# Optimization experiments

Measured on AMD Instinct MI355X. Metric: run time of the kernel, lower is better.

Reference implementation:

```python
import jax, jax.numpy as jnp
import numpy as np

B, G, K, KD = 16384, 17, 12, 16      # batch, games, kicks/game, kick feature dim
DK, DM, H, T = 16, 32, 2, 4          # d_kick, d_model, n_attn_heads, n_targets
SD, H1, H2, HH = 64, 256, 128, 32    # static_dim, backbone hidden dims, head hidden
AO = H * DM                          # attention output dim = 64
EPS = 1e-5
NEG_INF = float('-inf')


def setup_inputs() -> dict:
    ks = jax.random.split(jax.random.key(0), 18)
    n = lambda i, s, sc=0.05: jax.random.normal(ks[i], s, jnp.float32) * sc
    x_static = jax.random.normal(ks[0], (B, SD), jnp.float32)
    x_kicks = jax.random.normal(ks[1], (B, G, K, KD), jnp.float32)
    # masks: True = real game / kick; force position 0 valid so no row is fully padded
    outer_mask = jax.random.bernoulli(ks[2], 0.9, (B, G)).at[:, 0].set(True)
    inner_mask = jax.random.bernoulli(ks[3], 0.85, (B, G, K)).at[:, :, 0].set(True)
    return dict(
        x_static=x_static, x_kicks=x_kicks,
        W_ke=n(4, (KD, DK)), b_ke=jnp.zeros((DK,), jnp.float32),
        q_inner=n(5, (1, DK), 0.02),
        W_ge=n(6, (DK, DM)), b_ge=jnp.zeros((DM,), jnp.float32),
        pos_emb=n(7, (G, DM), 0.02),
        q_outer=n(8, (T * H, DM), 0.02),
        log_temp=jnp.zeros((T,), jnp.float32),
        ln_g=jnp.ones((T, AO), jnp.float32), ln_b=jnp.zeros((T, AO), jnp.float32),
        W1=n(9, (SD, H1)), b1=jnp.zeros((H1,), jnp.float32),
        g1=jnp.ones((H1,), jnp.float32), be1=jnp.zeros((H1,), jnp.float32),
        m1=n(10, (H1,)), v1=jax.random.uniform(ks[11], (H1,), jnp.float32) + 0.5,
        W2=n(12, (H1, H2)), b2=jnp.zeros((H2,), jnp.float32),
        g2=jnp.ones((H2,), jnp.float32), be2=jnp.zeros((H2,), jnp.float32),
        m2=n(13, (H2,)), v2=jax.random.uniform(ks[14], (H2,), jnp.float32) + 0.5,
        Wh1=n(15, (T, H2 + AO, HH)), bh1=jnp.zeros((T, HH), jnp.float32),
        Wh2=n(16, (T, HH)), bh2=jnp.zeros((T,), jnp.float32),
        outer_mask=outer_mask, inner_mask=inner_mask)


def _forward(x_static, x_kicks, W_ke, b_ke, q_inner, W_ge, b_ge, pos_emb,
             q_outer, log_temp, ln_g, ln_b, W1, b1, g1, be1, m1, v1,
             W2, b2, g2, be2, m2, v2, Wh1, bh1, Wh2, bh2,
             outer_mask, inner_mask):
    # kick encoder: Linear -> ReLU, [B,G,K,KD] -> [B,G,K,DK]
    kick_enc = jax.nn.relu(jnp.einsum('bgkd,de->bgke', x_kicks, W_ke) + b_ke)
    # inner AttentionPool: single learned query over kicks within each game
    ai = jnp.einsum('d,bgkd->bgk', q_inner[0], kick_enc) * (DK ** -0.5)
    ai = jnp.where(inner_mask, ai, NEG_INF)
    wi = jnp.nan_to_num(jax.nn.softmax(ai, axis=-1))       # all-masked rows -> 0
    per_game = jnp.einsum('bgk,bgkd->bgd', wi, kick_enc)   # [B,G,DK]
    # game encoder + learned positional embedding
    encoded = jax.nn.relu(per_game @ W_ge + b_ge) + pos_emb[None]  # [B,G,DM]
    # outer AttentionPool: T*H learned queries over games, per-target temperature
    ao = jnp.einsum('qd,bgd->bqg', q_outer, encoded) * (DM ** -0.5)
    ao = ao * jnp.repeat(jnp.exp(-log_temp), H)[None, :, None]
    ao = jnp.where(outer_mask[:, None, :], ao, NEG_INF)
    wo = jnp.nan_to_num(jax.nn.softmax(ao, axis=-1))
    pooled = jnp.einsum('bqg,bgd->bqd', wo, encoded).reshape(-1, T, AO)  # [B,T,64]
    # per-target LayerNorm on history vector
    mu = pooled.mean(-1, keepdims=True)
    var = ((pooled - mu) ** 2).mean(-1, keepdims=True)
    hist = (pooled - mu) * jax.lax.rsqrt(var + EPS) * ln_g[None] + ln_b[None]
    # backbone: Linear -> BatchNorm(eval) -> ReLU, x2 (dropout = identity in eval)
    z = jax.nn.relu((x_static @ W1 + b1 - m1) * jax.lax.rsqrt(v1 + EPS) * g1 + be1)
    z = jax.nn.relu((z @ W2 + b2 - m2) * jax.lax.rsqrt(v2 + EPS) * g2 + be2)
    # per-target heads on [shared_static ; history_vec]
    head_in = jnp.concatenate(
        [jnp.broadcast_to(z[:, None, :], (z.shape[0], T, H2)), hist], axis=-1)  # [B,T,192]
    h = jax.nn.relu(jnp.einsum('btd,tdh->bth', head_in, Wh1) + bh1[None])
    out = jnp.einsum('bth,th->bt', h, Wh2) + bh2[None]
    return jnp.maximum(out, 0.0)  # all targets non-negative (clamp, not softplus)


def reference(x_static, x_kicks, W_ke, b_ke, q_inner, W_ge, b_ge, pos_emb,
              q_outer, log_temp, ln_g, ln_b, W1, b1, g1, be1, m1, v1,
              W2, b2, g2, be2, m2, v2, Wh1, bh1, Wh2, bh2,
              outer_mask, inner_mask):
    return _forward(x_static, x_kicks, W_ke, b_ke, q_inner, W_ge, b_ge, pos_emb,
                    q_outer, log_temp, ln_g, ln_b, W1, b1, g1, be1, m1, v1,
                    W2, b2, g2, be2, m2, v2, Wh1, bh1, Wh2, bh2,
                    outer_mask, inner_mask)
```

## Files before the change

### kernel.cpp

```cpp
#include <hip/hip_runtime.h>
#include <math.h>

#define NEGM (-1e30f)

typedef __fp16 f16x4 __attribute__((ext_vector_type(4)));
typedef __fp16 f16x2 __attribute__((ext_vector_type(2)));
typedef float  f32x4 __attribute__((ext_vector_type(4)));

__device__ __forceinline__ float4 ld4(const float* p) { return *(const float4*)p; }
__device__ __forceinline__ void fma4(float4& a, float s, const float4 w) {
    a.x += s * w.x; a.y += s * w.y; a.z += s * w.z; a.w += s * w.w;
}

__global__ __launch_bounds__(64) void hist_kernel(
    const float* __restrict__ x_kicks,
    const float* __restrict__ W_ke, const float* __restrict__ b_ke,
    const float* __restrict__ q_inner,
    const float* __restrict__ W_ge, const float* __restrict__ b_ge,
    const float* __restrict__ pos_emb, const float* __restrict__ q_outer,
    const float* __restrict__ log_temp,
    const float* __restrict__ ln_g, const float* __restrict__ ln_b,
    const int* __restrict__ outer_mask, const int* __restrict__ inner_mask,
    float* __restrict__ hist)
{
    __shared__ float s_wge[512];
    __shared__ float s_qout[256];
    __shared__ float pg[17 * 20];
    __shared__ float enc[17 * 36];
    __shared__ float ao[136];
    __shared__ float s_S[20];

    const int lane = threadIdx.x;
    const int b    = blockIdx.x;
    const int jcol = lane & 15;
    const int g    = lane >> 4;
    const int kb   = g * 4;

    *(float4*)&s_wge[lane * 4]       = ld4(W_ge + lane * 4);
    *(float4*)&s_wge[256 + lane * 4] = ld4(W_ge + 256 + lane * 4);
    *(float4*)&s_qout[lane * 4]      = ld4(q_outer + lane * 4);

    f16x4 bw;
    #pragma unroll
    for (int jj = 0; jj < 4; ++jj)
        bw[jj] = (__fp16)W_ke[(kb + jj) * 16 + jcol];
    const float bias = b_ke[jcol];
    const f32x4 cinit = {bias, bias, bias, bias};
    const float qv = q_inner[jcol];

    const float* xb = x_kicks + (size_t)b * 204 * 16;
    const int*   mb = inner_mask + (size_t)b * 204;

    f32x4 PG   = {0.f, 0.f, 0.f, 0.f};
    f32x4 PG16 = {0.f, 0.f, 0.f, 0.f};
    float Sacc = 0.f, S16 = 0.f;

    #pragma unroll
    for (int t = 0; t < 12; ++t) {
        float4 xv = ld4(xb + (16 * t + jcol) * 16 + kb);
        f16x2 xlo = __builtin_amdgcn_cvt_pkrtz(xv.x, xv.y);
        f16x2 xhi = __builtin_amdgcn_cvt_pkrtz(xv.z, xv.w);
        f16x4 ax; ax[0] = xlo[0]; ax[1] = xlo[1]; ax[2] = xhi[0]; ax[3] = xhi[1];

        int4 mv = *(const int4*)(mb + 16 * t + 4 * g);

        f32x4 D1 = __builtin_amdgcn_mfma_f32_16x16x16f16(ax, bw, cinit, 0, 0, 0);
        #pragma unroll
        for (int jj = 0; jj < 4; ++jj) D1[jj] = fmaxf(D1[jj], 0.f);

        f32x4 ps;
        #pragma unroll
        for (int jj = 0; jj < 4; ++jj) ps[jj] = D1[jj] * qv;
        #pragma unroll
        for (int o = 1; o < 16; o <<= 1) {
            ps[0] += __shfl_xor(ps[0], o);
            ps[1] += __shfl_xor(ps[1], o);
            ps[2] += __shfl_xor(ps[2], o);
            ps[3] += __shfl_xor(ps[3], o);
        }

        f16x4 aw;
        #pragma unroll
        for (int jj = 0; jj < 4; ++jj) {
            int kk = 16 * t + 4 * g + jj;
            int mk = (jj == 0) ? mv.x : (jj == 1) ? mv.y : (jj == 2) ? mv.z : mv.w;
            float e = mk ? __expf(ps[jj] * 0.25f) : 0.f;
            float w = (kk / 12 == jcol) ? e : 0.f;
            aw[jj] = (__fp16)w;
            Sacc += w;
        }

        f16x2 elo = __builtin_amdgcn_cvt_pkrtz(D1[0], D1[1]);
        f16x2 ehi = __builtin_amdgcn_cvt_pkrtz(D1[2], D1[3]);
        f16x4 be; be[0] = elo[0]; be[1] = elo[1]; be[2] = ehi[0]; be[3] = ehi[1];

        PG = __builtin_amdgcn_mfma_f32_16x16x16f16(aw, be, PG, 0, 0, 0);
    }

    {
        int kidx = 192 + jcol;
        int kc = (kidx < 204) ? kidx : 203;
        float4 xv = ld4(xb + kc * 16 + kb);
        f16x2 xlo = __builtin_amdgcn_cvt_pkrtz(xv.x, xv.y);
        f16x2 xhi = __builtin_amdgcn_cvt_pkrtz(xv.z, xv.w);
        f16x4 ax; ax[0] = xlo[0]; ax[1] = xlo[1]; ax[2] = xhi[0]; ax[3] = xhi[1];

        int km = 192 + 4 * g;
        int kmc = (km <= 200) ? km : 200;
        int4 mv = *(const int4*)(mb + kmc);

        f32x4 D1 = __builtin_amdgcn_mfma_f32_16x16x16f16(ax, bw, cinit, 0, 0, 0);
        #pragma unroll
        for (int jj = 0; jj < 4; ++jj) D1[jj] = fmaxf(D1[jj], 0.f);

        f32x4 ps;
        #pragma unroll
        for (int jj = 0; jj < 4; ++jj) ps[jj] = D1[jj] * qv;
        #pragma unroll
        for (int o = 1; o < 16; o <<= 1) {
            ps[0] += __shfl_xor(ps[0], o);
            ps[1] += __shfl_xor(ps[1], o);
            ps[2] += __shfl_xor(ps[2], o);
            ps[3] += __shfl_xor(ps[3], o);
        }

        f16x4 aw2;
        #pragma unroll
        for (int jj = 0; jj < 4; ++jj) {
            int pos = 4 * g + jj;
            int mk = (jj == 0) ? mv.x : (jj == 1) ? mv.y : (jj == 2) ? mv.z : mv.w;
            bool valid = (pos < 12) && mk;
            float e = valid ? __expf(ps[jj] * 0.25f) : 0.f;
            float w = (jcol == 0) ? e : 0.f;
            aw2[jj] = (__fp16)w;
            S16 += w;
        }

        f16x2 elo = __builtin_amdgcn_cvt_pkrtz(D1[0], D1[1]);
        f16x2 ehi = __builtin_amdgcn_cvt_pkrtz(D1[2], D1[3]);
        f16x4 be; be[0] = elo[0]; be[1] = elo[1]; be[2] = ehi[0]; be[3] = ehi[1];

        PG16 = __builtin_amdgcn_mfma_f32_16x16x16f16(aw2, be, PG16, 0, 0, 0);
    }

    Sacc += __shfl_xor(Sacc, 16);
    Sacc += __shfl_xor(Sacc, 32);
    S16 += __shfl_xor(S16, 16);
    S16 += __shfl_xor(S16, 32);

    if (lane < 16) s_S[lane] = Sacc;
    if (lane == 0) s_S[16] = S16;
    __syncthreads();

    #pragma unroll
    for (int jj = 0; jj < 4; ++jj) {
        int game = kb + jj;
        pg[game * 20 + jcol] = PG[jj] * (1.f / s_S[game]);
    }
    if (lane < 16) pg[16 * 20 + lane] = PG16[0] * (1.f / s_S[16]);
    __syncthreads();

    for (int t = lane; t < 136; t += 64) {
        const int gg = t >> 3, dq = t & 7;
        float4 acc = ld4(b_ge + dq * 4);
        #pragma unroll
        for (int i = 0; i < 16; ++i) {
            float pv = pg[gg * 20 + i];
            fma4(acc, pv, *(float4*)&s_wge[i * 32 + dq * 4]);
        }
        float4 pe = ld4(pos_emb + gg * 32 + dq * 4);
        acc.x = fmaxf(acc.x, 0.f) + pe.x; acc.y = fmaxf(acc.y, 0.f) + pe.y;
        acc.z = fmaxf(acc.z, 0.f) + pe.z; acc.w = fmaxf(acc.w, 0.f) + pe.w;
        *(float4*)&enc[gg * 36 + dq * 4] = acc;
    }
    __syncthreads();

    for (int t = lane; t < 136; t += 64) {
        const int q = t / 17, gg = t - q * 17;
        float4 acc = {0.f, 0.f, 0.f, 0.f};
        #pragma unroll
        for (int i4 = 0; i4 < 8; ++i4) {
            float4 ev = *(float4*)&enc[gg * 36 + i4 * 4];
            float4 qvv = *(float4*)&s_qout[q * 32 + i4 * 4];
            acc.x += ev.x * qvv.x; acc.y += ev.y * qvv.y;
            acc.z += ev.z * qvv.z; acc.w += ev.w * qvv.w;
        }
        float sv = (acc.x + acc.y) + (acc.z + acc.w);
        sv *= 0.17677669529663687f * __expf(-log_temp[q >> 1]);
        ao[t] = outer_mask[b * 17 + gg] ? sv : NEGM;
    }
    __syncthreads();

    {
        const int q = lane >> 3, j = lane & 7;
        float s0 = ao[q * 17 + j];
        float s1 = ao[q * 17 + j + 8];
        float s2 = (j == 0) ? ao[q * 17 + 16] : NEGM;
        float mx = fmaxf(fmaxf(s0, s1), s2);
        mx = fmaxf(mx, __shfl_xor(mx, 1));
        mx = fmaxf(mx, __shfl_xor(mx, 2));
        mx = fmaxf(mx, __shfl_xor(mx, 4));
        float e0 = __expf(s0 - mx), e1 = __expf(s1 - mx);
        float e2 = (j == 0) ? __expf(s2 - mx) : 0.f;
        float ssum = e0 + e1 + e2;
        ssum += __shfl_xor(ssum, 1);
        ssum += __shfl_xor(ssum, 2);
        ssum += __shfl_xor(ssum, 4);
        float inv = 1.f / ssum;
        ao[q * 17 + j] = e0 * inv;
        ao[q * 17 + j + 8] = e1 * inv;
        if (j == 0) ao[q * 17 + 16] = e2 * inv;
    }
    __syncthreads();

    {
        const int q = lane >> 3, dq = lane & 7;
        float4 acc = {0.f, 0.f, 0.f, 0.f};
        #pragma unroll
        for (int gg = 0; gg < 17; ++gg) {
            float w = ao[q * 17 + gg];
            fma4(acc, w, *(float4*)&enc[gg * 36 + dq * 4]);
        }
        float sv = (acc.x + acc.y) + (acc.z + acc.w);
        sv += __shfl_xor(sv, 1); sv += __shfl_xor(sv, 2);
        sv += __shfl_xor(sv, 4); sv += __shfl_xor(sv, 8);
        float mu = sv * 0.015625f;
        float4 d;
        d.x = acc.x - mu; d.y = acc.y - mu; d.z = acc.z - mu; d.w = acc.w - mu;
        float v = (d.x * d.x + d.y * d.y) + (d.z * d.z + d.w * d.w);
        v += __shfl_xor(v, 1); v += __shfl_xor(v, 2);
        v += __shfl_xor(v, 4); v += __shfl_xor(v, 8);
        float rs = rsqrtf(v * 0.015625f + 1e-5f);
        float4 gam = ld4(ln_g + lane * 4);
        float4 bet = ld4(ln_b + lane * 4);
        float4 res;
        res.x = d.x * rs * gam.x + bet.x; res.y = d.y * rs * gam.y + bet.y;
        res.z = d.z * rs * gam.z + bet.z; res.w = d.w * rs * gam.w + bet.w;
        *(float4*)&hist[(size_t)b * 256 + lane * 4] = res;
    }
}

__global__ __launch_bounds__(256) void backbone_kernel(
    const float* __restrict__ x_static,
    const float* __restrict__ W1, const float* __restrict__ b1,
    const float* __restrict__ g1, const float* __restrict__ be1,
    const float* __restrict__ m1, const float* __restrict__ v1,
    const float* __restrict__ W2, const float* __restrict__ b2,
    const float* __restrict__ g2, const float* __restrict__ be2,
    const float* __restrict__ m2, const float* __restrict__ v2,
    const float* __restrict__ Wh1, const float* __restrict__ bh1,
    const float* __restrict__ Wh2, const float* __restrict__ bh2,
    const float* __restrict__ hist, float* __restrict__ out)
{
    __shared__ float s_x[16 * 64];
    __shared__ float s_z1[16 * 256];
    __shared__ float s_z2[16 * 132];

    const int tid = threadIdx.x;
    const int row0 = blockIdx.x * 16;

    *(float4*)&s_x[tid * 4] = ld4(x_static + (size_t)row0 * 64 + tid * 4);
    __syncthreads();

    {
        const int col = tid;
        float acc[16];
        #pragma unroll
        for (int r = 0; r < 16; ++r) acc[r] = 0.f;
        for (int k4 = 0; k4 < 16; ++k4) {
            float w0 = W1[(k4 * 4 + 0) * 256 + col];
            float w1 = W1[(k4 * 4 + 1) * 256 + col];
            float w2 = W1[(k4 * 4 + 2) * 256 + col];
            float w3 = W1[(k4 * 4 + 3) * 256 + col];
            #pragma unroll
            for (int r = 0; r < 16; ++r) {
                float4 xv = *(float4*)&s_x[r * 64 + k4 * 4];
                acc[r] += xv.x * w0 + xv.y * w1 + xv.z * w2 + xv.w * w3;
            }
        }
        float sc = rsqrtf(v1[col] + 1e-5f) * g1[col];
        float off = b1[col] - m1[col];
        float bb = be1[col];
        #pragma unroll
        for (int r = 0; r < 16; ++r)
            s_z1[r * 256 + col] = fmaxf((acc[r] + off) * sc + bb, 0.f);
    }
    __syncthreads();

    {
        const int col = tid & 127;
        const int r0 = (tid >> 7) * 8;
        float acc[8];
        #pragma unroll
        for (int r = 0; r < 8; ++r) acc[r] = 0.f;
        for (int k4 = 0; k4 < 64; ++k4) {
            float w0 = W2[(k4 * 4 + 0) * 128 + col];
            float w1 = W2[(k4 * 4 + 1) * 128 + col];
            float w2 = W2[(k4 * 4 + 2) * 128 + col];
            float w3 = W2[(k4 * 4 + 3) * 128 + col];
            #pragma unroll
            for (int r = 0; r < 8; ++r) {
                float4 zv = *(float4*)&s_z1[(r0 + r) * 256 + k4 * 4];
                acc[r] += zv.x * w0 + zv.y * w1 + zv.z * w2 + zv.w * w3;
            }
        }
        float sc = rsqrtf(v2[col] + 1e-5f) * g2[col];
        float off = b2[col] - m2[col];
        float bb = be2[col];
        #pragma unroll
        for (int r = 0; r < 8; ++r)
            s_z2[(r0 + r) * 132 + col] = fmaxf((acc[r] + off) * sc + bb, 0.f);
    }
    __syncthreads();

    {
        const int p = tid >> 2;
        const int gl = tid & 3;
        const int row = p >> 2;
        const int tgt = p & 3;
        const int j0 = gl * 8;

        float acc[8];
        #pragma unroll
        for (int j = 0; j < 8; ++j) acc[j] = bh1[tgt * 32 + j0 + j];

        const float* w1p = Wh1 + (size_t)tgt * 192 * 32 + j0;
        for (int d4 = 0; d4 < 32; ++d4) {
            float4 zv = *(float4*)&s_z2[row * 132 + d4 * 4];
            #pragma unroll
            for (int c = 0; c < 4; ++c) {
                float v = (c == 0) ? zv.x : (c == 1) ? zv.y : (c == 2) ? zv.z : zv.w;
                float4 a = ld4(w1p + (d4 * 4 + c) * 32);
                float4 bq = ld4(w1p + (d4 * 4 + c) * 32 + 4);
                acc[0] += v * a.x;  acc[1] += v * a.y;  acc[2] += v * a.z;  acc[3] += v * a.w;
                acc[4] += v * bq.x; acc[5] += v * bq.y; acc[6] += v * bq.z; acc[7] += v * bq.w;
            }
        }
        const float* hp = hist + (size_t)(row0 + row) * 256 + tgt * 64;
        const float* w1q = w1p + 128 * 32;
        for (int d4 = 0; d4 < 16; ++d4) {
            float4 hv = ld4(hp + d4 * 4);
            #pragma unroll
            for (int c = 0; c < 4; ++c) {
                float v = (c == 0) ? hv.x : (c == 1) ? hv.y : (c == 2) ? hv.z : hv.w;
                float4 a = ld4(w1q + (d4 * 4 + c) * 32);
                float4 bq = ld4(w1q + (d4 * 4 + c) * 32 + 4);
                acc[0] += v * a.x;  acc[1] += v * a.y;  acc[2] += v * a.z;  acc[3] += v * a.w;
                acc[4] += v * bq.x; acc[5] += v * bq.y; acc[6] += v * bq.z; acc[7] += v * bq.w;
            }
        }
        float ps = 0.f;
        #pragma unroll
        for (int j = 0; j < 8; ++j) ps += fmaxf(acc[j], 0.f) * Wh2[tgt * 32 + j0 + j];
        ps += __shfl_xor(ps, 1);
        ps += __shfl_xor(ps, 2);
        if (gl == 0) out[(size_t)(row0 + row) * 4 + tgt] = fmaxf(ps + bh2[tgt], 0.f);
    }
}

extern "C" void kernel_launch(void* const* d_in, const int* in_sizes, int n_in,
                              void* d_out, int out_size, void* d_ws, size_t ws_size,
                              hipStream_t stream) {
    const float* x_static = (const float*)d_in[0];
    const float* x_kicks  = (const float*)d_in[1];
    const float* W_ke     = (const float*)d_in[2];
    const float* b_ke     = (const float*)d_in[3];
    const float* q_inner  = (const float*)d_in[4];
    const float* W_ge     = (const float*)d_in[5];
    const float* b_ge     = (const float*)d_in[6];
    const float* pos_emb  = (const float*)d_in[7];
    const float* q_outer  = (const float*)d_in[8];
    const float* log_temp = (const float*)d_in[9];
    const float* ln_g     = (const float*)d_in[10];
    const float* ln_b     = (const float*)d_in[11];
    const float* W1       = (const float*)d_in[12];
    const float* b1       = (const float*)d_in[13];
    const float* g1       = (const float*)d_in[14];
    const float* be1      = (const float*)d_in[15];
    const float* m1       = (const float*)d_in[16];
    const float* v1       = (const float*)d_in[17];
    const float* W2       = (const float*)d_in[18];
    const float* b2       = (const float*)d_in[19];
    const float* g2       = (const float*)d_in[20];
    const float* be2      = (const float*)d_in[21];
    const float* m2       = (const float*)d_in[22];
    const float* v2       = (const float*)d_in[23];
    const float* Wh1      = (const float*)d_in[24];
    const float* bh1      = (const float*)d_in[25];
    const float* Wh2      = (const float*)d_in[26];
    const float* bh2      = (const float*)d_in[27];
    const int* outer_mask = (const int*)d_in[28];
    const int* inner_mask = (const int*)d_in[29];

    float* hist = (float*)d_ws;
    float* out  = (float*)d_out;

    hist_kernel<<<16384, 64, 0, stream>>>(
        x_kicks, W_ke, b_ke, q_inner, W_ge, b_ge, pos_emb, q_outer,
        log_temp, ln_g, ln_b, outer_mask, inner_mask, hist);

    backbone_kernel<<<16384 / 16, 256, 0, stream>>>(
        x_static, W1, b1, g1, be1, m1, v1, W2, b2, g2, be2, m2, v2,
        Wh1, bh1, Wh2, bh2, hist, out);
}
```

Measured before the change: 145.5 us.

## Split history kernel into MFMA pooling and outer-attention kernels

The single per-sample history kernel becomes two kernels. A pooling kernel packs four samples per 256-thread block with no shared memory and writes normalized pooled game vectors to a workspace. A second kernel packs two samples per block and runs the game encoder, outer attention and layer norm. The aim is higher occupancy and less block-scheduling overhead for the bandwidth-bound kick pass, at the cost of an extra global round-trip of about 17 MB of intermediates and one more kernel launch.

```diff
diff --git a/kernel.cpp b/kernel.cpp
--- a/kernel.cpp
+++ b/kernel.cpp
@@ -12,33 +12,20 @@
     a.x += s * w.x; a.y += s * w.y; a.z += s * w.z; a.w += s * w.w;
 }
 
-__global__ __launch_bounds__(64) void hist_kernel(
+__global__ __launch_bounds__(256, 8) void pool_kernel(
     const float* __restrict__ x_kicks,
     const float* __restrict__ W_ke, const float* __restrict__ b_ke,
     const float* __restrict__ q_inner,
-    const float* __restrict__ W_ge, const float* __restrict__ b_ge,
-    const float* __restrict__ pos_emb, const float* __restrict__ q_outer,
-    const float* __restrict__ log_temp,
-    const float* __restrict__ ln_g, const float* __restrict__ ln_b,
-    const int* __restrict__ outer_mask, const int* __restrict__ inner_mask,
-    float* __restrict__ hist)
+    const int* __restrict__ inner_mask,
+    float* __restrict__ pg_out)
 {
-    __shared__ float s_wge[512];
-    __shared__ float s_qout[256];
-    __shared__ float pg[17 * 20];
-    __shared__ float enc[17 * 36];
-    __shared__ float ao[136];
-    __shared__ float s_S[20];
-
-    const int lane = threadIdx.x;
-    const int b    = blockIdx.x;
+    const int tid  = threadIdx.x;
+    const int wid  = tid >> 6;
+    const int lane = tid & 63;
+    const int b    = blockIdx.x * 4 + wid;
     const int jcol = lane & 15;
     const int g    = lane >> 4;
     const int kb   = g * 4;
-
-    *(float4*)&s_wge[lane * 4]       = ld4(W_ge + lane * 4);
-    *(float4*)&s_wge[256 + lane * 4] = ld4(W_ge + 256 + lane * 4);
-    *(float4*)&s_qout[lane * 4]      = ld4(q_outer + lane * 4);
 
     f16x4 bw;
     #pragma unroll
@@ -51,18 +38,16 @@
     const float* xb = x_kicks + (size_t)b * 204 * 16;
     const int*   mb = inner_mask + (size_t)b * 204;
 
-    f32x4 PG   = {0.f, 0.f, 0.f, 0.f};
-    f32x4 PG16 = {0.f, 0.f, 0.f, 0.f};
+    f32x4 PG = {0,0,0,0}, PG16 = {0,0,0,0};
     float Sacc = 0.f, S16 = 0.f;
 
-    #pragma unroll
     for (int t = 0; t < 12; ++t) {
         float4 xv = ld4(xb + (16 * t + jcol) * 16 + kb);
+        int4 mv = *(const int4*)(mb + 16 * t + 4 * g);
+
         f16x2 xlo = __builtin_amdgcn_cvt_pkrtz(xv.x, xv.y);
         f16x2 xhi = __builtin_amdgcn_cvt_pkrtz(xv.z, xv.w);
-        f16x4 ax; ax[0] = xlo[0]; ax[1] = xlo[1]; ax[2] = xhi[0]; ax[3] = xhi[1];
-
-        int4 mv = *(const int4*)(mb + 16 * t + 4 * g);
+        f16x4 ax; ax[0]=xlo[0]; ax[1]=xlo[1]; ax[2]=xhi[0]; ax[3]=xhi[1];
 
         f32x4 D1 = __builtin_amdgcn_mfma_f32_16x16x16f16(ax, bw, cinit, 0, 0, 0);
         #pragma unroll
@@ -83,7 +68,7 @@
         #pragma unroll
         for (int jj = 0; jj < 4; ++jj) {
             int kk = 16 * t + 4 * g + jj;
-            int mk = (jj == 0) ? mv.x : (jj == 1) ? mv.y : (jj == 2) ? mv.z : mv.w;
+            int mk = (jj==0)?mv.x:(jj==1)?mv.y:(jj==2)?mv.z:mv.w;
             float e = mk ? __expf(ps[jj] * 0.25f) : 0.f;
             float w = (kk / 12 == jcol) ? e : 0.f;
             aw[jj] = (__fp16)w;
@@ -92,7 +77,7 @@
 
         f16x2 elo = __builtin_amdgcn_cvt_pkrtz(D1[0], D1[1]);
         f16x2 ehi = __builtin_amdgcn_cvt_pkrtz(D1[2], D1[3]);
-        f16x4 be; be[0] = elo[0]; be[1] = elo[1]; be[2] = ehi[0]; be[3] = ehi[1];
+        f16x4 be; be[0]=elo[0]; be[1]=elo[1]; be[2]=ehi[0]; be[3]=ehi[1];
 
         PG = __builtin_amdgcn_mfma_f32_16x16x16f16(aw, be, PG, 0, 0, 0);
     }
@@ -101,13 +86,13 @@
         int kidx = 192 + jcol;
         int kc = (kidx < 204) ? kidx : 203;
         float4 xv = ld4(xb + kc * 16 + kb);
-        f16x2 xlo = __builtin_amdgcn_cvt_pkrtz(xv.x, xv.y);
-        f16x2 xhi = __builtin_amdgcn_cvt_pkrtz(xv.z, xv.w);
-        f16x4 ax; ax[0] = xlo[0]; ax[1] = xlo[1]; ax[2] = xhi[0]; ax[3] = xhi[1];
-
         int km = 192 + 4 * g;
         int kmc = (km <= 200) ? km : 200;
         int4 mv = *(const int4*)(mb + kmc);
+
+        f16x2 xlo = __builtin_amdgcn_cvt_pkrtz(xv.x, xv.y);
+        f16x2 xhi = __builtin_amdgcn_cvt_pkrtz(xv.z, xv.w);
+        f16x4 ax; ax[0]=xlo[0]; ax[1]=xlo[1]; ax[2]=xhi[0]; ax[3]=xhi[1];
 
         f32x4 D1 = __builtin_amdgcn_mfma_f32_16x16x16f16(ax, bw, cinit, 0, 0, 0);
         #pragma unroll
@@ -128,7 +113,7 @@
         #pragma unroll
         for (int jj = 0; jj < 4; ++jj) {
             int pos = 4 * g + jj;
-            int mk = (jj == 0) ? mv.x : (jj == 1) ? mv.y : (jj == 2) ? mv.z : mv.w;
+            int mk = (jj==0)?mv.x:(jj==1)?mv.y:(jj==2)?mv.z:mv.w;
             bool valid = (pos < 12) && mk;
             float e = valid ? __expf(ps[jj] * 0.25f) : 0.f;
             float w = (jcol == 0) ? e : 0.f;
@@ -138,7 +123,7 @@
 
         f16x2 elo = __builtin_amdgcn_cvt_pkrtz(D1[0], D1[1]);
         f16x2 ehi = __builtin_amdgcn_cvt_pkrtz(D1[2], D1[3]);
-        f16x4 be; be[0] = elo[0]; be[1] = elo[1]; be[2] = ehi[0]; be[3] = ehi[1];
+        f16x4 be; be[0]=elo[0]; be[1]=elo[1]; be[2]=ehi[0]; be[3]=ehi[1];
 
         PG16 = __builtin_amdgcn_mfma_f32_16x16x16f16(aw2, be, PG16, 0, 0, 0);
     }
@@ -147,47 +132,89 @@
     Sacc += __shfl_xor(Sacc, 32);
     S16 += __shfl_xor(S16, 16);
     S16 += __shfl_xor(S16, 32);
-
-    if (lane < 16) s_S[lane] = Sacc;
-    if (lane == 0) s_S[16] = S16;
-    __syncthreads();
-
+    float S16all = __shfl(S16, 0);
+
+    float* op = pg_out + (size_t)b * 272;
     #pragma unroll
     for (int jj = 0; jj < 4; ++jj) {
         int game = kb + jj;
-        pg[game * 20 + jcol] = PG[jj] * (1.f / s_S[game]);
-    }
-    if (lane < 16) pg[16 * 20 + lane] = PG16[0] * (1.f / s_S[16]);
-    __syncthreads();
+        float Sg = __shfl(Sacc, game);
+        op[game * 16 + jcol] = PG[jj] * (1.f / Sg);
+    }
+    if (lane < 16) op[256 + lane] = PG16[0] * (1.f / S16all);
+}
+
+__global__ __launch_bounds__(128) void histbe_kernel(
+    const float* __restrict__ pg_in,
+    const float* __restrict__ W_ge, const float* __restrict__ b_ge,
+    const float* __restrict__ pos_emb, const float* __restrict__ q_outer,
+    const float* __restrict__ log_temp,
+    const float* __restrict__ ln_g, const float* __restrict__ ln_b,
+    const int* __restrict__ outer_mask,
+    float* __restrict__ hist)
+{
+    __shared__ float s_wge[512];
+    __shared__ float s_qout[256];
+    __shared__ float s_pg[2][17 * 20];
+    __shared__ float s_enc[2][17 * 36];
+    __shared__ float s_ao[2][136];
+
+    const int tid  = threadIdx.x;
+    const int wid  = tid >> 6;
+    const int lane = tid & 63;
+    const int b    = blockIdx.x * 2 + wid;
+
+    s_qout[tid] = q_outer[tid];
+    s_qout[tid + 128] = q_outer[tid + 128];
+    s_wge[tid] = W_ge[tid];
+    s_wge[tid + 128] = W_ge[tid + 128];
+    s_wge[tid + 256] = W_ge[tid + 256];
+    s_wge[tid + 384] = W_ge[tid + 384];
+
+    {
+        const float* pgb = pg_in + (size_t)b * 272;
+        float4 v = ld4(pgb + lane * 4);
+        const int g = lane >> 2, d = (lane & 3) * 4;
+        *(float4*)&s_pg[wid][g * 20 + d] = v;
+        if (lane < 4) {
+            float4 v2 = ld4(pgb + 256 + lane * 4);
+            *(float4*)&s_pg[wid][16 * 20 + lane * 4] = v2;
+        }
+    }
+    __syncthreads();
+
+    float* pg  = s_pg[wid];
+    float* enc = s_enc[wid];
+    float* ao  = s_ao[wid];
 
     for (int t = lane; t < 136; t += 64) {
-        const int gg = t >> 3, dq = t & 7;
+        const int g = t >> 3, dq = t & 7;
         float4 acc = ld4(b_ge + dq * 4);
         #pragma unroll
         for (int i = 0; i < 16; ++i) {
-            float pv = pg[gg * 20 + i];
+            float pv = pg[g * 20 + i];
             fma4(acc, pv, *(float4*)&s_wge[i * 32 + dq * 4]);
         }
-        float4 pe = ld4(pos_emb + gg * 32 + dq * 4);
+        float4 pe = ld4(pos_emb + g * 32 + dq * 4);
         acc.x = fmaxf(acc.x, 0.f) + pe.x; acc.y = fmaxf(acc.y, 0.f) + pe.y;
         acc.z = fmaxf(acc.z, 0.f) + pe.z; acc.w = fmaxf(acc.w, 0.f) + pe.w;
-        *(float4*)&enc[gg * 36 + dq * 4] = acc;
+        *(float4*)&enc[g * 36 + dq * 4] = acc;
     }
     __syncthreads();
 
     for (int t = lane; t < 136; t += 64) {
-        const int q = t / 17, gg = t - q * 17;
+        const int q = t / 17, g = t - q * 17;
         float4 acc = {0.f, 0.f, 0.f, 0.f};
         #pragma unroll
         for (int i4 = 0; i4 < 8; ++i4) {
-            float4 ev = *(float4*)&enc[gg * 36 + i4 * 4];
-            float4 qvv = *(float4*)&s_qout[q * 32 + i4 * 4];
-            acc.x += ev.x * qvv.x; acc.y += ev.y * qvv.y;
-            acc.z += ev.z * qvv.z; acc.w += ev.w * qvv.w;
+            float4 ev = *(float4*)&enc[g * 36 + i4 * 4];
+            float4 qv = *(float4*)&s_qout[q * 32 + i4 * 4];
+            acc.x += ev.x * qv.x; acc.y += ev.y * qv.y;
+            acc.z += ev.z * qv.z; acc.w += ev.w * qv.w;
         }
         float sv = (acc.x + acc.y) + (acc.z + acc.w);
         sv *= 0.17677669529663687f * __expf(-log_temp[q >> 1]);
-        ao[t] = outer_mask[b * 17 + gg] ? sv : NEGM;
+        ao[t] = outer_mask[b * 17 + g] ? sv : NEGM;
     }
     __syncthreads();
 
@@ -217,9 +244,9 @@
         const int q = lane >> 3, dq = lane & 7;
         float4 acc = {0.f, 0.f, 0.f, 0.f};
         #pragma unroll
-        for (int gg = 0; gg < 17; ++gg) {
-            float w = ao[q * 17 + gg];
-            fma4(acc, w, *(float4*)&enc[gg * 36 + dq * 4]);
+        for (int g = 0; g < 17; ++g) {
+            float w = ao[q * 17 + g];
+            fma4(acc, w, *(float4*)&enc[g * 36 + dq * 4]);
         }
         float sv = (acc.x + acc.y) + (acc.z + acc.w);
         sv += __shfl_xor(sv, 1); sv += __shfl_xor(sv, 2);
@@ -392,12 +419,16 @@
     const int* outer_mask = (const int*)d_in[28];
     const int* inner_mask = (const int*)d_in[29];
 
-    float* hist = (float*)d_ws;
+    float* pg   = (float*)d_ws;
+    float* hist = pg + (size_t)16384 * 272;
     float* out  = (float*)d_out;
 
-    hist_kernel<<<16384, 64, 0, stream>>>(
-        x_kicks, W_ke, b_ke, q_inner, W_ge, b_ge, pos_emb, q_outer,
-        log_temp, ln_g, ln_b, outer_mask, inner_mask, hist);
+    pool_kernel<<<16384 / 4, 256, 0, stream>>>(
+        x_kicks, W_ke, b_ke, q_inner, inner_mask, pg);
+
+    histbe_kernel<<<16384 / 2, 128, 0, stream>>>(
+        pg, W_ge, b_ge, pos_emb, q_outer, log_temp, ln_g, ln_b,
+        outer_mask, hist);
 
     backbone_kernel<<<16384 / 16, 256, 0, stream>>>(
         x_static, W1, b1, g1, be1, m1, v1, W2, b2, g2, be2, m2, v2,
```

Result: slower. 152.4 us (+4.8%).
